# Kernel tuning notes

Measured on AMD Instinct MI355X. Metric: run time of the kernel, lower is better.

The kernel has to match this reference:

```python
import jax, jax.numpy as jnp
import numpy as np

S, T, D_OUT = 64, 256, 64
B = 64
HEADS = 2
D0 = S + T              # 320
D1 = D0 * (1 + HEADS)   # 960
D2 = D1 * (1 + HEADS)   # 2880
PARAM_SCALE = 0.02


def setup_inputs() -> dict:
    key = jax.random.key(0)
    k1, k2, k3, k4 = jax.random.split(key, 4)
    x = jax.random.normal(k1, (B, T, S), dtype=jnp.float32)
    A0 = jax.random.normal(k2, (HEADS, D0, D0), dtype=jnp.float32) * PARAM_SCALE
    A1 = jax.random.normal(k3, (HEADS, D1, D1), dtype=jnp.float32) * PARAM_SCALE
    Wo = jax.random.normal(k4, (D_OUT, D2), dtype=jnp.float32) * PARAM_SCALE
    return {"x": x, "A0": A0, "A1": A1, "Wo": Wo}


def _causal_self_attention(h, A):
    # h: [B, T, d], A: [H, d, d]
    Bsz, Tlen, d = h.shape
    H = A.shape[0]
    # bilinear scores per head: h @ A[i] @ h^T, vectorized over heads
    scores = jnp.einsum('btd,hde,bse->bhts', h, A, h)  # [B, H, T, T]
    neg_inf = jnp.asarray(float('-inf'), dtype=h.dtype)
    mask = jnp.triu(jnp.full((Tlen, Tlen), neg_inf, dtype=h.dtype), k=1)
    attn = jax.nn.softmax(scores + mask, axis=-1)
    out = jnp.einsum('bhts,bsd->bthd', attn, h)  # [B, T, H, d]
    return out.reshape(Bsz, Tlen, H * d)


def reference(x, A0, A1, Wo):
    Bsz, Tlen, _ = x.shape
    # one-hot positional encoding concatenated onto input
    pos = jnp.broadcast_to(jnp.eye(Tlen, dtype=x.dtype)[None], (Bsz, Tlen, Tlen))
    h = jnp.concatenate([x, pos], axis=-1)          # [B, T, S+T]
    h = jnp.concatenate([h, _causal_self_attention(h, A0)], axis=-1)  # [B, T, D1]
    h = jnp.concatenate([h, _causal_self_attention(h, A1)], axis=-1)  # [B, T, D2]
    logits = jnp.einsum('btd,od->bto', h, Wo)       # [B, T, d_out]
    return logits
```

## Files before the change

kernel.cpp:

```cpp
#include <hip/hip_runtime.h>
#include <math.h>

#define NB 64
#define NT 256
#define NS 64
#define ND0 320
#define ND1 960
#define ND2 2880
#define NH 2
#define DC 704

typedef __attribute__((ext_vector_type(8))) _Float16 f16x8;
typedef __attribute__((ext_vector_type(4))) float f32x4;
typedef __attribute__((ext_vector_type(4))) short short4v;

typedef const __attribute__((address_space(1))) void* gas_ptr;
typedef __attribute__((address_space(3))) void* las_ptr;
#define GLOAD16(g, l) __builtin_amdgcn_global_load_lds((gas_ptr)(g), (las_ptr)(l), 16, 0, 0)
#define MFMAH(a, b, c) __builtin_amdgcn_mfma_f32_16x16x32_f16((a), (b), (c), 0, 0, 0)

__device__ __forceinline__ short f2h(float v) {
    union { _Float16 h; short s; } u; u.h = (_Float16)v; return u.s;
}
__device__ __forceinline__ float h2f(short b) {
    union { _Float16 h; short s; } u; u.s = b; return (float)u.h;
}
__device__ __forceinline__ int swz(int o) { return o ^ (((o >> 7) & 7) << 4); }

__global__ __launch_bounds__(256, 2) void gemmG1(
    const short* __restrict__ hc,
    const short* __restrict__ At,
    short* __restrict__ G,
    const float* __restrict__ A1)
{
    int wg = blockIdx.x;
    int q8 = gridDim.x >> 3;
    int sid = (wg & 7) * q8 + (wg >> 3);
    int bx = sid % 15, by = sid / 15;
    int m0 = by << 8, n0 = bx << 7;

    __shared__ short lds[24576];
    int tid = threadIdx.x;
    int lane = tid & 63, w = tid >> 6;
    int wm = w >> 1, wn = w & 1;
    int q = lane >> 4, l15 = lane & 15;

    const short* aS[8]; const short* bS[4];
    int dA[8], dB[4];
#pragma unroll
    for (int j = 0; j < 8; ++j) {
        int o = j * 4096 + tid * 16;
        int c = swz(o); int r = c >> 7, col = (c & 127) >> 1;
        aS[j] = hc + (long)(m0 + r) * DC + col;
        dA[j] = o >> 1;
    }
#pragma unroll
    for (int j = 0; j < 4; ++j) {
        int o = j * 4096 + tid * 16;
        int c = swz(o); int r = c >> 7, col = (c & 127) >> 1;
        bS[j] = At + (long)(n0 + r) * DC + col;
        dB[j] = o >> 1;
    }

    int oa[8][2], ob[4][2];
#pragma unroll
    for (int mf = 0; mf < 8; ++mf)
#pragma unroll
        for (int kf = 0; kf < 2; ++kf) {
            int row = wm * 128 + mf * 16 + l15;
            oa[mf][kf] = swz(row * 128 + (kf * 32 + (q << 3)) * 2) >> 1;
        }
#pragma unroll
    for (int nf = 0; nf < 4; ++nf)
#pragma unroll
        for (int kf = 0; kf < 2; ++kf) {
            int row = wn * 64 + nf * 16 + l15;
            ob[nf][kf] = swz(row * 128 + (kf * 32 + (q << 3)) * 2) >> 1;
        }

    f32x4 acc[8][4] = {};

    for (int k0 = 0; k0 < DC; k0 += 64) {
#pragma unroll
        for (int j = 0; j < 8; ++j) { GLOAD16(aS[j], lds + dA[j]); aS[j] += 64; }
#pragma unroll
        for (int j = 0; j < 4; ++j) { GLOAD16(bS[j], lds + 16384 + dB[j]); bS[j] += 64; }
        __syncthreads();
#pragma unroll
        for (int kf = 0; kf < 2; ++kf) {
            f16x8 vb[4];
#pragma unroll
            for (int nf = 0; nf < 4; ++nf)
                vb[nf] = *(const f16x8*)(lds + 16384 + ob[nf][kf]);
#pragma unroll
            for (int mf = 0; mf < 8; ++mf) {
                f16x8 va = *(const f16x8*)(lds + oa[mf][kf]);
#pragma unroll
                for (int nf = 0; nf < 4; ++nf)
                    acc[mf][nf] = MFMAH(va, vb[nf], acc[mf][nf]);
            }
        }
        __syncthreads();
    }

#pragma unroll
    for (int mf = 0; mf < 8; ++mf)
#pragma unroll
        for (int nf = 0; nf < 4; ++nf) {
            int col = n0 + wn * 64 + nf * 16 + l15;
            int head = (col >= 960) ? 1 : 0;
            int colh = col - head * 960;
            const float* bA = A1 + (long)head * 921600 + colh;
            int rowb = m0 + wm * 128 + mf * 16 + (q << 2);
#pragma unroll
            for (int r = 0; r < 4; ++r) {
                int t = (rowb + r) & 255;
                float f = acc[mf][nf][r] + bA[(long)(64 + t) * 960];
                G[(long)(rowb + r) * 1920 + col] = f2h(f);
            }
        }
}

template <int CMODE, int TERMS, bool AJUMP>
__global__ __launch_bounds__(256, 3) void gemm128(
    const short* Ah, int lda, long sA,
    const short* Bh, const short* Bl, int ldb, long sB,
    float* Cf, int ldcf, long sCf,
    const short* biasH, long ldbias,
    long hsA, long hsC,
    int K)
{
    int bx = blockIdx.x, by = blockIdx.y;
    int m0 = by * 128, n0 = bx * 128;
    if (CMODE == 0 && n0 > m0 + 127) return;
    long zLo = blockIdx.z & 63, zHi = blockIdx.z >> 6;
    const short* pAh = Ah + zLo * sA + zHi * hsA;
    const short* pBh = Bh + zLo * sB;
    const short* pBl = (TERMS == 2) ? (Bl + zLo * sB) : nullptr;

    __shared__ short lds[8192 * (1 + TERMS)];
    short* LAh = lds;
    short* LBh = lds + 8192;
    short* LBl = lds + 16384;

    int tid = threadIdx.x;
    int lane = tid & 63, w = tid >> 6;
    int wr = w >> 1, wc = w & 1;

    const short* aSH[4]; const short* bSH[4]; const short* bSL[4];
    int aLo[4], bLo[4];
#pragma unroll
    for (int j = 0; j < 4; ++j) {
        int o = j * 4096 + tid * 16;
        int c = swz(o); int r = c >> 7, col = (c & 127) >> 1;
        aSH[j] = pAh + (long)(m0 + r) * lda + col;
        aLo[j] = o >> 1;
        bSH[j] = pBh + (long)(n0 + r) * ldb + col;
        if (TERMS == 2) bSL[j] = pBl + (long)(n0 + r) * ldb + col;
        bLo[j] = o >> 1;
    }

    int oa[4][2], ob[4][2];
#pragma unroll
    for (int mf = 0; mf < 4; ++mf)
#pragma unroll
        for (int kf = 0; kf < 2; ++kf) {
            int row = wr * 64 + mf * 16 + (lane & 15);
            oa[mf][kf] = swz(row * 128 + (kf * 32 + ((lane >> 4) << 3)) * 2) >> 1;
        }
#pragma unroll
    for (int nf = 0; nf < 4; ++nf)
#pragma unroll
        for (int kf = 0; kf < 2; ++kf) {
            int row = wc * 64 + nf * 16 + (lane & 15);
            ob[nf][kf] = swz(row * 128 + (kf * 32 + ((lane >> 4) << 3)) * 2) >> 1;
        }

    f32x4 acc[4][4] = {};

    for (int k0 = 0; k0 < K; k0 += 64) {
        int step = (AJUMP && k0 == 0) ? 320 : 64;
#pragma unroll
        for (int j = 0; j < 4; ++j) {
            GLOAD16(aSH[j], LAh + aLo[j]);
            aSH[j] += step;
            GLOAD16(bSH[j], LBh + bLo[j]);
            bSH[j] += 64;
            if (TERMS == 2) { GLOAD16(bSL[j], LBl + bLo[j]); bSL[j] += 64; }
        }
        __syncthreads();
#pragma unroll
        for (int kf = 0; kf < 2; ++kf) {
            f16x8 vbh[4], vbl[4];
#pragma unroll
            for (int nf = 0; nf < 4; ++nf) {
                vbh[nf] = *(const f16x8*)(LBh + ob[nf][kf]);
                if (TERMS == 2) vbl[nf] = *(const f16x8*)(LBl + ob[nf][kf]);
            }
#pragma unroll
            for (int mf = 0; mf < 4; ++mf) {
                f16x8 vah = *(const f16x8*)(LAh + oa[mf][kf]);
#pragma unroll
                for (int nf = 0; nf < 4; ++nf) {
                    acc[mf][nf] = MFMAH(vah, vbh[nf], acc[mf][nf]);
                    if (TERMS == 2) acc[mf][nf] = MFMAH(vah, vbl[nf], acc[mf][nf]);
                }
            }
        }
        __syncthreads();
    }

#pragma unroll
    for (int mf = 0; mf < 4; ++mf)
#pragma unroll
        for (int nf = 0; nf < 4; ++nf) {
            f32x4 v = acc[mf][nf];
            int col  = n0 + wc * 64 + nf * 16 + (lane & 15);
            int rowb = m0 + wr * 64 + mf * 16 + ((lane >> 4) << 2);
#pragma unroll
            for (int r = 0; r < 4; ++r) {
                long o = (zLo * 256 + rowb + r) * ldbias + 64 + col + zHi * hsA;
                v[r] += h2f(biasH[o]);
            }
#pragma unroll
            for (int r = 0; r < 4; ++r)
                Cf[zLo * sCf + zHi * hsC + (long)(rowb + r) * ldcf + col] = v[r];
        }
}

template <int BMODE, int TERMS, bool KCAUSAL, bool ACC, bool OUTU, bool BJUMP>
__global__ __launch_bounds__(256) void gemm_mfma(
    const short* Ah, int lda, long sA,
    const short* Bh, const short* Bl, int ldb, long sB, long hsB,
    float* Cf, int ldcf, long sCf,
    short* Chi, short* Clo, int ldch, long sCh,
    const float* biasF, long ldbias, long hsBias,
    long hsA, long hsC,
    short* UThi,
    int K)
{
    int m0 = blockIdx.y * 128, n0 = blockIdx.x * 64;
    long zLo = blockIdx.z & 63, zHi = blockIdx.z >> 6;
    const short* pAh = Ah + zLo * sA + zHi * hsA;
    const short* pBh = Bh + zLo * sB + zHi * hsB;
    const short* pBl = (TERMS == 2) ? (Bl + zLo * sB + zHi * hsB) : nullptr;

    __shared__ short lds[8192 + TERMS * 4096];
    short* LAh = lds;
    short* LBh = lds + 8192;
    short* LBl = lds + 12288;

    int tid = threadIdx.x;
    int lane = tid & 63, w = tid >> 6;
    int wr = w >> 1, wc = w & 1;

    const short* aSH[4]; const short* bSH[2]; const short* bSL[2];
    int aLo[4], bLo[2];
#pragma unroll
    for (int j = 0; j < 4; ++j) {
        int o = j * 4096 + tid * 16;
        int c = swz(o); int r = c >> 7, col = (c & 127) >> 1;
        aSH[j] = pAh + (long)(m0 + r) * lda + col;
        aLo[j] = o >> 1;
    }
#pragma unroll
    for (int j = 0; j < 2; ++j) {
        int o = j * 4096 + tid * 16;
        int c = swz(o); int r = c >> 7, col = (c & 127) >> 1;
        bSH[j] = pBh + (long)(n0 + r) * ldb + col;
        if (TERMS == 2) bSL[j] = pBl + (long)(n0 + r) * ldb + col;
        bLo[j] = o >> 1;
    }

    int oa[4][2], ob[2][2];
#pragma unroll
    for (int mf = 0; mf < 4; ++mf)
#pragma unroll
        for (int kf = 0; kf < 2; ++kf) {
            int row = wr * 64 + mf * 16 + (lane & 15);
            oa[mf][kf] = swz(row * 128 + (kf * 32 + ((lane >> 4) << 3)) * 2) >> 1;
        }
#pragma unroll
    for (int nf = 0; nf < 2; ++nf)
#pragma unroll
        for (int kf = 0; kf < 2; ++kf) {
            int row = wc * 32 + nf * 16 + (lane & 15);
            ob[nf][kf] = swz(row * 128 + (kf * 32 + ((lane >> 4) << 3)) * 2) >> 1;
        }

    f32x4 acc[4][2] = {};
    int Klim = KCAUSAL ? (K < m0 + 128 ? K : m0 + 128) : K;

    for (int k0 = 0; k0 < Klim; k0 += 64) {
#pragma unroll
        for (int j = 0; j < 4; ++j) {
            GLOAD16(aSH[j], LAh + aLo[j]);
            aSH[j] += 64;
        }
        long bstep = (BJUMP && k0 == 192) ? (1048576L - 192L) : 64L;
#pragma unroll
        for (int j = 0; j < 2; ++j) {
            GLOAD16(bSH[j], LBh + bLo[j]);
            bSH[j] += bstep;
            if (TERMS == 2) { GLOAD16(bSL[j], LBl + bLo[j]); bSL[j] += bstep; }
        }
        __syncthreads();
#pragma unroll
        for (int kf = 0; kf < 2; ++kf) {
            f16x8 vbh[2], vbl[2];
#pragma unroll
            for (int nf = 0; nf < 2; ++nf) {
                vbh[nf] = *(const f16x8*)(LBh + ob[nf][kf]);
                if (TERMS == 2) vbl[nf] = *(const f16x8*)(LBl + ob[nf][kf]);
            }
#pragma unroll
            for (int mf = 0; mf < 4; ++mf) {
                f16x8 vah = *(const f16x8*)(LAh + oa[mf][kf]);
#pragma unroll
                for (int nf = 0; nf < 2; ++nf) {
                    acc[mf][nf] = MFMAH(vah, vbh[nf], acc[mf][nf]);
                    if (TERMS == 2) acc[mf][nf] = MFMAH(vah, vbl[nf], acc[mf][nf]);
                }
            }
        }
        __syncthreads();
    }

#pragma unroll
    for (int mf = 0; mf < 4; ++mf)
#pragma unroll
        for (int nf = 0; nf < 2; ++nf) {
            f32x4 v = acc[mf][nf];
            int col  = n0 + wc * 32 + nf * 16 + (lane & 15);
            int rowb = m0 + wr * 64 + mf * 16 + ((lane >> 4) << 2);
            if (BMODE == 1) {
#pragma unroll
                for (int r = 0; r < 4; ++r) {
                    int t = (rowb + r) & 255;
                    v[r] += biasF[zLo * hsBias + (long)(64 + t) * ldbias + col];
                }
            } else if (BMODE == 3) {
#pragma unroll
                for (int r = 0; r < 4; ++r) {
                    int t = (rowb + r) & 255;
                    v[r] += biasF[(long)(col - n0) * 2880 + (n0 >> 6) * 960 + 64 + t];
                }
            }
            if (OUTU) {
                if (n0 == 0) {
#pragma unroll
                    for (int r = 0; r < 4; ++r)
                        Cf[(long)(rowb + r) * ldcf + col] = v[r];
                } else {
                    int head = (n0 >> 6) - 1;
                    int o = col - n0;
                    short hs[4];
#pragma unroll
                    for (int r = 0; r < 4; ++r) hs[r] = f2h(v[r]);
                    short4v th = {hs[0], hs[1], hs[2], hs[3]};
                    *(short4v*)(UThi + head * 1048576L + (long)o * 16384 + rowb) = th;
                }
            } else if (ACC) {
#pragma unroll
                for (int r = 0; r < 4; ++r)
                    Cf[zLo * sCf + (long)(rowb + r) * ldcf + col] += v[r];
            } else if (Cf) {
#pragma unroll
                for (int r = 0; r < 4; ++r)
                    Cf[zLo * sCf + (long)(rowb + r) * ldcf + col] = v[r];
            } else {
#pragma unroll
                for (int r = 0; r < 4; ++r) {
                    float f = v[r];
                    short hi = f2h(f);
                    Chi[zHi * hsC + zLo * sCh + (long)(rowb + r) * ldch + col] = hi;
                    if (Clo)
                        Clo[zHi * hsC + zLo * sCh + (long)(rowb + r) * ldch + col] = f2h(f - h2f(hi));
                }
            }
        }
}

__global__ __launch_bounds__(256) void build_h_rows(const float* __restrict__ x,
                                                    short* __restrict__ hhi) {
    int idx = blockIdx.x * 256 + threadIdx.x;
    int bt = idx >> 6, c = idx & 63;
    hhi[(long)bt * DC + c] = f2h(x[(long)bt * NS + c]);
}

__global__ __launch_bounds__(256) void build_hT_x(const float* __restrict__ x,
                                                  short* __restrict__ hTh) {
    __shared__ float tile[32][33];
    int c0 = blockIdx.x * 32, t0 = blockIdx.y * 32, b = blockIdx.z;
    int tx = threadIdx.x, ty = threadIdx.y;
    const float* xb = x + (long)b * NT * NS;
#pragma unroll
    for (int i = ty; i < 32; i += 8) tile[i][tx] = xb[(long)(t0 + i) * NS + c0 + tx];
    __syncthreads();
    long base = (long)b * (NS * 256);
#pragma unroll
    for (int i = ty; i < 32; i += 8)
        hTh[base + (long)(c0 + i) * 256 + t0 + tx] = f2h(tile[tx][i]);
}

__global__ void build_At(const float* __restrict__ A,
                         short* __restrict__ hi,
                         int dN, int dK, int srcLd, int shift, int dSrcN) {
    __shared__ float tile[32][33];
    int k0 = blockIdx.x * 32, n0 = blockIdx.y * 32;
    long hbase = (long)blockIdx.z * srcLd * srcLd;
    int tx = threadIdx.x, ty = threadIdx.y;
#pragma unroll
    for (int i = ty; i < 32; i += 8) {
        int k = k0 + i;
        int srck = (k < 64) ? k : k + shift;
        tile[i][tx] = (n0 + tx < dSrcN) ? A[hbase + (long)srck * srcLd + n0 + tx] : 0.f;
    }
    __syncthreads();
    long obase = (long)blockIdx.z * dN * dK;
#pragma unroll
    for (int i = ty; i < 32; i += 8)
        hi[obase + (long)(n0 + i) * dK + k0 + tx] = f2h(tile[tx][i]);
}

__global__ __launch_bounds__(256) void build_Wf(const float* __restrict__ Wo,
                                                short* __restrict__ hi) {
    int idx = blockIdx.x * 256 + threadIdx.x;
    if (idx >= 192 * DC) return;
    int r = idx / DC, kc = idx - r * DC;
    int o = r & 63, chunk = r >> 6;
    int srck = (kc < 64) ? kc : kc + 256;
    hi[idx] = f2h(Wo[(long)o * ND2 + chunk * 960 + srck]);
}

__global__ __launch_bounds__(256) void softmax_split(const float* S,
                                                     short* pHi,
                                                     int ldo, long hs) {
    int row  = blockIdx.x * 4 + (threadIdx.x >> 6);
    int t    = row & (NT - 1);
    int hrow = row & 16383;
    int head = row >> 14;
    int lane = threadIdx.x & 63;
    int s0   = lane << 2;
    const float* p = S + (long)row * NT;

    float4 v = *(const float4*)(p + s0);
    float vv[4] = {v.x, v.y, v.z, v.w};
    float mx = -INFINITY;
#pragma unroll
    for (int j = 0; j < 4; ++j)
        if (s0 + j <= t) mx = fmaxf(mx, vv[j]);
    for (int off = 32; off; off >>= 1) mx = fmaxf(mx, __shfl_down(mx, off));
    mx = __shfl(mx, 0);

    float e[4]; float sum = 0.f;
#pragma unroll
    for (int j = 0; j < 4; ++j) {
        e[j] = (s0 + j <= t) ? __expf(vv[j] - mx) : 0.f;
        sum += e[j];
    }
    for (int off = 32; off; off >>= 1) sum += __shfl_down(sum, off);
    sum = __shfl(sum, 0);
    float inv = 1.f / sum;

    short hsv[4];
#pragma unroll
    for (int j = 0; j < 4; ++j) hsv[j] = f2h(e[j] * inv);
    short4v hv = {hsv[0], hsv[1], hsv[2], hsv[3]};
    *(short4v*)(pHi + (long)head * hs + (long)hrow * ldo + s0) = hv;
}

__global__ __launch_bounds__(256) void build_h0(const float* __restrict__ x,
                                                float* __restrict__ h) {
    int idx = blockIdx.x * 256 + threadIdx.x;
    int bt = idx / ND0;
    int c  = idx - bt * ND0;
    int t  = bt & (NT - 1);
    float v;
    if (c < NS) v = x[(long)bt * NS + c];
    else        v = ((c - NS) == t) ? 1.0f : 0.0f;
    h[(long)bt * ND2 + c] = v;
}

template <bool BT, bool CAUSAL>
__global__ __launch_bounds__(256) void gemm64(
    const float* __restrict__ A, int lda, long sA,
    const float* __restrict__ Bm, int ldb, long sB,
    float* __restrict__ C, int ldc, long sC, int K)
{
    int m0 = blockIdx.y * 64, n0 = blockIdx.x * 64;
    if (CAUSAL && n0 > m0 + 63) return;
    long z = blockIdx.z;
    A += z * sA; Bm += z * sB; C += z * sC;

    __shared__ float As[16][68];
    __shared__ float Bs[16][68];

    int tid = threadIdx.x;
    int tx = tid & 15, ty = tid >> 4;
    int rowA = tid >> 2, kA = (tid & 3) << 2;
    int kB = tid >> 4,  colB = (tid & 15) << 2;

    float acc[4][4] = {};

    for (int k0 = 0; k0 < K; k0 += 16) {
        float4 av = *(const float4*)(A + (long)(m0 + rowA) * lda + k0 + kA);
        As[kA + 0][rowA] = av.x; As[kA + 1][rowA] = av.y;
        As[kA + 2][rowA] = av.z; As[kA + 3][rowA] = av.w;
        if (BT) {
            float4 bv = *(const float4*)(Bm + (long)(n0 + rowA) * ldb + k0 + kA);
            Bs[kA + 0][rowA] = bv.x; Bs[kA + 1][rowA] = bv.y;
            Bs[kA + 2][rowA] = bv.z; Bs[kA + 3][rowA] = bv.w;
        } else {
            float4 bv = *(const float4*)(Bm + (long)(k0 + kB) * ldb + n0 + colB);
            *(float4*)(&Bs[kB][colB]) = bv;
        }
        __syncthreads();
#pragma unroll
        for (int kk = 0; kk < 16; ++kk) {
            float4 a4 = *(const float4*)(&As[kk][ty << 2]);
            float4 b4 = *(const float4*)(&Bs[kk][tx << 2]);
            float a[4] = {a4.x, a4.y, a4.z, a4.w};
            float b[4] = {b4.x, b4.y, b4.z, b4.w};
#pragma unroll
            for (int i = 0; i < 4; ++i)
#pragma unroll
                for (int j = 0; j < 4; ++j)
                    acc[i][j] += a[i] * b[j];
        }
        __syncthreads();
    }
#pragma unroll
    for (int i = 0; i < 4; ++i) {
        float4 v = {acc[i][0], acc[i][1], acc[i][2], acc[i][3]};
        *(float4*)(C + (long)(m0 + (ty << 2) + i) * ldc + n0 + (tx << 2)) = v;
    }
}

__global__ __launch_bounds__(256) void softmax_causal(float* __restrict__ P) {
    int row  = blockIdx.x * 4 + (threadIdx.x >> 6);
    int t    = row & (NT - 1);
    int lane = threadIdx.x & 63;
    int s0   = lane << 2;
    float* p = P + (long)row * NT;

    float4 v = *(const float4*)(p + s0);
    float vv[4] = {v.x, v.y, v.z, v.w};
    float mx = -INFINITY;
#pragma unroll
    for (int j = 0; j < 4; ++j)
        if (s0 + j <= t) mx = fmaxf(mx, vv[j]);
    for (int off = 32; off; off >>= 1) mx = fmaxf(mx, __shfl_down(mx, off));
    mx = __shfl(mx, 0);

    float e[4]; float sum = 0.f;
#pragma unroll
    for (int j = 0; j < 4; ++j) {
        e[j] = (s0 + j <= t) ? __expf(vv[j] - mx) : 0.f;
        sum += e[j];
    }
    for (int off = 32; off; off >>= 1) sum += __shfl_down(sum, off);
    sum = __shfl(sum, 0);
    float inv = 1.f / sum;
    float4 o = {e[0] * inv, e[1] * inv, e[2] * inv, e[3] * inv};
    *(float4*)(p + s0) = o;
}

extern "C" void kernel_launch(void* const* d_in, const int* in_sizes, int n_in,
                              void* d_out, int out_size, void* d_ws, size_t ws_size,
                              hipStream_t stream) {
    const float* x  = (const float*)d_in[0];
    const float* A0 = (const float*)d_in[1];
    const float* A1 = (const float*)d_in[2];
    const float* Wo = (const float*)d_in[3];
    float* out = (float*)d_out;

    if (ws_size >= 175120384UL) {
        char* wsb = (char*)d_ws;
        short* hc_hi = (short*)(wsb);
        short* G_hi  = (short*)(wsb + 46137344L);
        float* S     = (float*)(wsb + 113246208L);
        short* P     = (short*)(wsb + 146800640L);
        short* hT_hi = (short*)(wsb + 163577856L);
        short* At_hi = (short*)(wsb + 167772160L);
        short* Wf_hi = (short*)(wsb + 170655744L);
        short* UT_hi = (short*)(wsb + 170926080L);

        build_h_rows<<<4096, 256, 0, stream>>>(x, hc_hi);
        build_hT_x<<<dim3(2, 8, 64), dim3(32, 8), 0, stream>>>(x, hT_hi);
        build_Wf<<<528, 256, 0, stream>>>(Wo, Wf_hi);

        build_At<<<dim3(2, 10, 2), dim3(32, 8), 0, stream>>>(A0, At_hi, ND0, 64, ND0, 0, ND0);
        gemm_mfma<1, 1, false, false, false, false><<<dim3(5, 128, 2), 256, 0, stream>>>(
            hc_hi, DC, 0L,
            At_hi, nullptr, 64, 20480L, 0L,
            nullptr, 0, 0L, G_hi, nullptr, 640, 320L,
            A0, 320L, 102400L,
            0L, 0L,
            nullptr, 64);
        gemm128<0, 1, false><<<dim3(2, 2, 128), 256, 0, stream>>>(
            G_hi, 640, 163840L,
            hc_hi, nullptr, DC, 180224L,
            S, NT, 65536L,
            G_hi, 640L,
            320L, 4194304L, 64);
        softmax_split<<<8192, 256, 0, stream>>>(S, hc_hi + 128, DC, 320L);
        gemm_mfma<0, 1, true, false, false, false><<<dim3(1, 2, 128), 256, 0, stream>>>(
            hc_hi + 128, DC, 180224L,
            hT_hi, nullptr, 256, 16384L, 0L,
            nullptr, 0, 0L,
            hc_hi + 64, nullptr, DC, 180224L,
            nullptr, 0L, 0L,
            320L, 320L,
            nullptr, 256);

        gemm_mfma<3, 1, false, false, true, false><<<dim3(3, 128, 1), 256, 0, stream>>>(
            hc_hi, DC, 0L,
            Wf_hi, nullptr, DC, 0L, 0L,
            out, NS, 0L, nullptr, nullptr, 0, 0L,
            Wo, 0L, 0L,
            0L, 0L,
            UT_hi, DC);

        build_At<<<dim3(22, 30, 2), dim3(32, 8), 0, stream>>>(A1, At_hi, 960, DC, ND1, 256, ND1);
        gemmG1<<<960, 256, 0, stream>>>(hc_hi, At_hi, G_hi, A1);
        gemm128<0, 1, true><<<dim3(2, 2, 128), 256, 0, stream>>>(
            G_hi, 1920, 491520L,
            hc_hi, nullptr, DC, 180224L,
            S, NT, 65536L,
            G_hi, 1920L,
            960L, 4194304L, DC);
        softmax_split<<<8192, 256, 0, stream>>>(S, P, 512, 256L);
        gemm_mfma<0, 1, false, true, false, true><<<dim3(1, 2, 64), 256, 0, stream>>>(
            P, 512, 131072L,
            UT_hi, nullptr, 16384, 256L, 0L,
            out, NS, 16384L, nullptr, nullptr, 0, 0L,
            nullptr, 0L, 0L,
            0L, 0L,
            nullptr, 512);
        return;
    }

    float* ws = (float*)d_ws;
    float* h  = ws;
    float* G  = ws + 47185920L;
    float* Pf = ws + 47185920L + 15728640L;

    build_h0<<<(NB * NT * ND0) / 256, 256, 0, stream>>>(x, h);

    for (int layer = 0; layer < 2; ++layer) {
        int d = layer ? ND1 : ND0;
        const float* Am = layer ? A1 : A0;
        for (int head = 0; head < NH; ++head) {
            const float* Ah = Am + (long)head * d * d;
            gemm64<false, false><<<dim3(d / 64, 256, 1), 256, 0, stream>>>(
                h, ND2, 0L, Ah, d, 0L, G, d, 0L, d);
            gemm64<true, true><<<dim3(4, 4, NB), 256, 0, stream>>>(
                G, d, (long)NT * d, h, ND2, (long)NT * ND2,
                Pf, NT, (long)NT * NT, d);
            softmax_causal<<<(NB * NT) / 4, 256, 0, stream>>>(Pf);
            gemm64<false, false><<<dim3(d / 64, 4, NB), 256, 0, stream>>>(
                Pf, NT, (long)NT * NT, h, ND2, (long)NT * ND2,
                h + (long)d * (1 + head), ND2, (long)NT * ND2, NT);
        }
    }
    gemm64<true, false><<<dim3(1, 256, 1), 256, 0, stream>>>(
        h, ND2, 0L, Wo, ND2, 0L, out, NS, 0L, ND2);
}
```

Before: 177.5 us.

## Double-buffer gemmG1, store scores in fp16, fuse setup kernels, drop split-term paths

gemmG1 now stages K in 32-wide chunks into two LDS buffers and prefetches the next chunk while MFMAs run on the current one, which removes one barrier per step and hides load latency. Attention scores S are written and read as fp16 instead of fp32, halving the score traffic between the GEMM and softmax. The four setup kernels (h rows, x transpose, Wf, A0 transpose) are merged into one launch to cut launch overhead, and the unused lo-term template paths are removed. Storing scores in fp16 adds rounding before softmax, and large logits could lose accuracy or overflow.

```diff
diff --git a/kernel.cpp b/kernel.cpp
--- a/kernel.cpp
+++ b/kernel.cpp
@@ -45,63 +45,69 @@
     int wm = w >> 1, wn = w & 1;
     int q = lane >> 4, l15 = lane & 15;
 
-    const short* aS[8]; const short* bS[4];
-    int dA[8], dB[4];
-#pragma unroll
-    for (int j = 0; j < 8; ++j) {
-        int o = j * 4096 + tid * 16;
-        int c = swz(o); int r = c >> 7, col = (c & 127) >> 1;
-        aS[j] = hc + (long)(m0 + r) * DC + col;
-        dA[j] = o >> 1;
-    }
+    const short* aS[4]; const short* bS[2];
+    int dA[4], dB[2];
 #pragma unroll
     for (int j = 0; j < 4; ++j) {
         int o = j * 4096 + tid * 16;
-        int c = swz(o); int r = c >> 7, col = (c & 127) >> 1;
-        bS[j] = At + (long)(n0 + r) * DC + col;
+        int c = swz(o);
+        int sr = c >> 7, byt = c & 127;
+        int row = sr * 2 + (byt >> 6), k = (byt & 63) >> 1;
+        aS[j] = hc + (long)(m0 + row) * DC + k;
+        dA[j] = o >> 1;
+    }
+#pragma unroll
+    for (int j = 0; j < 2; ++j) {
+        int o = j * 4096 + tid * 16;
+        int c = swz(o);
+        int sr = c >> 7, byt = c & 127;
+        int row = sr * 2 + (byt >> 6), k = (byt & 63) >> 1;
+        bS[j] = At + (long)(n0 + row) * DC + k;
         dB[j] = o >> 1;
     }
 
-    int oa[8][2], ob[4][2];
-#pragma unroll
-    for (int mf = 0; mf < 8; ++mf)
-#pragma unroll
-        for (int kf = 0; kf < 2; ++kf) {
-            int row = wm * 128 + mf * 16 + l15;
-            oa[mf][kf] = swz(row * 128 + (kf * 32 + (q << 3)) * 2) >> 1;
-        }
-#pragma unroll
-    for (int nf = 0; nf < 4; ++nf)
-#pragma unroll
-        for (int kf = 0; kf < 2; ++kf) {
-            int row = wn * 64 + nf * 16 + l15;
-            ob[nf][kf] = swz(row * 128 + (kf * 32 + (q << 3)) * 2) >> 1;
-        }
+#define STG(BUF) { \
+    GLOAD16(aS[0], lds + (BUF) + dA[0]); GLOAD16(aS[1], lds + (BUF) + dA[1]); \
+    GLOAD16(aS[2], lds + (BUF) + dA[2]); GLOAD16(aS[3], lds + (BUF) + dA[3]); \
+    GLOAD16(bS[0], lds + (BUF) + 8192 + dB[0]); GLOAD16(bS[1], lds + (BUF) + 8192 + dB[1]); \
+    aS[0] += 32; aS[1] += 32; aS[2] += 32; aS[3] += 32; bS[0] += 32; bS[1] += 32; }
+
+    int oa[8], ob[4];
+#pragma unroll
+    for (int mf = 0; mf < 8; ++mf) {
+        int row = wm * 128 + mf * 16 + l15;
+        int sr = row >> 1, half = row & 1;
+        oa[mf] = swz(sr * 128 + half * 64 + q * 16) >> 1;
+    }
+#pragma unroll
+    for (int nf = 0; nf < 4; ++nf) {
+        int row = wn * 64 + nf * 16 + l15;
+        int sr = row >> 1, half = row & 1;
+        ob[nf] = swz(sr * 128 + half * 64 + q * 16) >> 1;
+    }
 
     f32x4 acc[8][4] = {};
 
-    for (int k0 = 0; k0 < DC; k0 += 64) {
-#pragma unroll
-        for (int j = 0; j < 8; ++j) { GLOAD16(aS[j], lds + dA[j]); aS[j] += 64; }
-#pragma unroll
-        for (int j = 0; j < 4; ++j) { GLOAD16(bS[j], lds + 16384 + dB[j]); bS[j] += 64; }
-        __syncthreads();
-#pragma unroll
-        for (int kf = 0; kf < 2; ++kf) {
-            f16x8 vb[4];
+    STG(0)
+    __syncthreads();
+#pragma unroll 2
+    for (int t = 0; t < 22; ++t) {
+        int cur = (t & 1) * 12288;
+        if (t < 21) STG(12288 - cur)
+        f16x8 vb[4];
+#pragma unroll
+        for (int nf = 0; nf < 4; ++nf)
+            vb[nf] = *(const f16x8*)(lds + cur + 8192 + ob[nf]);
+#pragma unroll
+        for (int mf = 0; mf < 8; ++mf) {
+            f16x8 va = *(const f16x8*)(lds + cur + oa[mf]);
 #pragma unroll
             for (int nf = 0; nf < 4; ++nf)
-                vb[nf] = *(const f16x8*)(lds + 16384 + ob[nf][kf]);
-#pragma unroll
-            for (int mf = 0; mf < 8; ++mf) {
-                f16x8 va = *(const f16x8*)(lds + oa[mf][kf]);
-#pragma unroll
-                for (int nf = 0; nf < 4; ++nf)
-                    acc[mf][nf] = MFMAH(va, vb[nf], acc[mf][nf]);
-            }
-        }
-        __syncthreads();
-    }
+                acc[mf][nf] = MFMAH(va, vb[nf], acc[mf][nf]);
+        }
+        __syncthreads();
+    }
+#undef STG
 
 #pragma unroll
     for (int mf = 0; mf < 8; ++mf)
@@ -121,33 +127,31 @@
         }
 }
 
-template <int CMODE, int TERMS, bool AJUMP>
+template <bool AJUMP>
 __global__ __launch_bounds__(256, 3) void gemm128(
     const short* Ah, int lda, long sA,
-    const short* Bh, const short* Bl, int ldb, long sB,
-    float* Cf, int ldcf, long sCf,
+    const short* Bh, int ldb, long sB,
+    short* Sf, int ldcf, long sCf,
     const short* biasH, long ldbias,
     long hsA, long hsC,
     int K)
 {
     int bx = blockIdx.x, by = blockIdx.y;
     int m0 = by * 128, n0 = bx * 128;
-    if (CMODE == 0 && n0 > m0 + 127) return;
+    if (n0 > m0 + 127) return;
     long zLo = blockIdx.z & 63, zHi = blockIdx.z >> 6;
     const short* pAh = Ah + zLo * sA + zHi * hsA;
     const short* pBh = Bh + zLo * sB;
-    const short* pBl = (TERMS == 2) ? (Bl + zLo * sB) : nullptr;
-
-    __shared__ short lds[8192 * (1 + TERMS)];
+
+    __shared__ short lds[16384];
     short* LAh = lds;
     short* LBh = lds + 8192;
-    short* LBl = lds + 16384;
 
     int tid = threadIdx.x;
     int lane = tid & 63, w = tid >> 6;
     int wr = w >> 1, wc = w & 1;
 
-    const short* aSH[4]; const short* bSH[4]; const short* bSL[4];
+    const short* aSH[4]; const short* bSH[4];
     int aLo[4], bLo[4];
 #pragma unroll
     for (int j = 0; j < 4; ++j) {
@@ -156,7 +160,6 @@
         aSH[j] = pAh + (long)(m0 + r) * lda + col;
         aLo[j] = o >> 1;
         bSH[j] = pBh + (long)(n0 + r) * ldb + col;
-        if (TERMS == 2) bSL[j] = pBl + (long)(n0 + r) * ldb + col;
         bLo[j] = o >> 1;
     }
 
@@ -186,25 +189,20 @@
             aSH[j] += step;
             GLOAD16(bSH[j], LBh + bLo[j]);
             bSH[j] += 64;
-            if (TERMS == 2) { GLOAD16(bSL[j], LBl + bLo[j]); bSL[j] += 64; }
         }
         __syncthreads();
 #pragma unroll
         for (int kf = 0; kf < 2; ++kf) {
-            f16x8 vbh[4], vbl[4];
-#pragma unroll
-            for (int nf = 0; nf < 4; ++nf) {
+            f16x8 vbh[4];
+#pragma unroll
+            for (int nf = 0; nf < 4; ++nf)
                 vbh[nf] = *(const f16x8*)(LBh + ob[nf][kf]);
-                if (TERMS == 2) vbl[nf] = *(const f16x8*)(LBl + ob[nf][kf]);
-            }
 #pragma unroll
             for (int mf = 0; mf < 4; ++mf) {
                 f16x8 vah = *(const f16x8*)(LAh + oa[mf][kf]);
 #pragma unroll
-                for (int nf = 0; nf < 4; ++nf) {
+                for (int nf = 0; nf < 4; ++nf)
                     acc[mf][nf] = MFMAH(vah, vbh[nf], acc[mf][nf]);
-                    if (TERMS == 2) acc[mf][nf] = MFMAH(vah, vbl[nf], acc[mf][nf]);
-                }
             }
         }
         __syncthreads();
@@ -224,16 +222,16 @@
             }
 #pragma unroll
             for (int r = 0; r < 4; ++r)
-                Cf[zLo * sCf + zHi * hsC + (long)(rowb + r) * ldcf + col] = v[r];
-        }
-}
-
-template <int BMODE, int TERMS, bool KCAUSAL, bool ACC, bool OUTU, bool BJUMP>
+                Sf[zLo * sCf + zHi * hsC + (long)(rowb + r) * ldcf + col] = f2h(v[r]);
+        }
+}
+
+template <int BMODE, bool KCAUSAL, bool ACC, bool OUTU, bool BJUMP>
 __global__ __launch_bounds__(256) void gemm_mfma(
     const short* Ah, int lda, long sA,
-    const short* Bh, const short* Bl, int ldb, long sB, long hsB,
+    const short* Bh, int ldb, long sB, long hsB,
     float* Cf, int ldcf, long sCf,
-    short* Chi, short* Clo, int ldch, long sCh,
+    short* Chi, int ldch, long sCh,
     const float* biasF, long ldbias, long hsBias,
     long hsA, long hsC,
     short* UThi,
@@ -243,18 +241,16 @@
     long zLo = blockIdx.z & 63, zHi = blockIdx.z >> 6;
     const short* pAh = Ah + zLo * sA + zHi * hsA;
     const short* pBh = Bh + zLo * sB + zHi * hsB;
-    const short* pBl = (TERMS == 2) ? (Bl + zLo * sB + zHi * hsB) : nullptr;
-
-    __shared__ short lds[8192 + TERMS * 4096];
+
+    __shared__ short lds[12288];
     short* LAh = lds;
     short* LBh = lds + 8192;
-    short* LBl = lds + 12288;
 
     int tid = threadIdx.x;
     int lane = tid & 63, w = tid >> 6;
     int wr = w >> 1, wc = w & 1;
 
-    const short* aSH[4]; const short* bSH[2]; const short* bSL[2];
+    const short* aSH[4]; const short* bSH[2];
     int aLo[4], bLo[2];
 #pragma unroll
     for (int j = 0; j < 4; ++j) {
@@ -268,7 +264,6 @@
         int o = j * 4096 + tid * 16;
         int c = swz(o); int r = c >> 7, col = (c & 127) >> 1;
         bSH[j] = pBh + (long)(n0 + r) * ldb + col;
-        if (TERMS == 2) bSL[j] = pBl + (long)(n0 + r) * ldb + col;
         bLo[j] = o >> 1;
     }
 
@@ -302,25 +297,20 @@
         for (int j = 0; j < 2; ++j) {
             GLOAD16(bSH[j], LBh + bLo[j]);
             bSH[j] += bstep;
-            if (TERMS == 2) { GLOAD16(bSL[j], LBl + bLo[j]); bSL[j] += bstep; }
         }
         __syncthreads();
 #pragma unroll
         for (int kf = 0; kf < 2; ++kf) {
-            f16x8 vbh[2], vbl[2];
-#pragma unroll
-            for (int nf = 0; nf < 2; ++nf) {
+            f16x8 vbh[2];
+#pragma unroll
+            for (int nf = 0; nf < 2; ++nf)
                 vbh[nf] = *(const f16x8*)(LBh + ob[nf][kf]);
-                if (TERMS == 2) vbl[nf] = *(const f16x8*)(LBl + ob[nf][kf]);
-            }
 #pragma unroll
             for (int mf = 0; mf < 4; ++mf) {
                 f16x8 vah = *(const f16x8*)(LAh + oa[mf][kf]);
 #pragma unroll
-                for (int nf = 0; nf < 2; ++nf) {
+                for (int nf = 0; nf < 2; ++nf)
                     acc[mf][nf] = MFMAH(vah, vbh[nf], acc[mf][nf]);
-                    if (TERMS == 2) acc[mf][nf] = MFMAH(vah, vbl[nf], acc[mf][nf]);
-                }
             }
         }
         __syncthreads();
@@ -370,37 +360,62 @@
                     Cf[zLo * sCf + (long)(rowb + r) * ldcf + col] = v[r];
             } else {
 #pragma unroll
-                for (int r = 0; r < 4; ++r) {
-                    float f = v[r];
-                    short hi = f2h(f);
-                    Chi[zHi * hsC + zLo * sCh + (long)(rowb + r) * ldch + col] = hi;
-                    if (Clo)
-                        Clo[zHi * hsC + zLo * sCh + (long)(rowb + r) * ldch + col] = f2h(f - h2f(hi));
-                }
+                for (int r = 0; r < 4; ++r)
+                    Chi[zHi * hsC + zLo * sCh + (long)(rowb + r) * ldch + col] = f2h(v[r]);
             }
         }
 }
 
-__global__ __launch_bounds__(256) void build_h_rows(const float* __restrict__ x,
-                                                    short* __restrict__ hhi) {
-    int idx = blockIdx.x * 256 + threadIdx.x;
-    int bt = idx >> 6, c = idx & 63;
-    hhi[(long)bt * DC + c] = f2h(x[(long)bt * NS + c]);
-}
-
-__global__ __launch_bounds__(256) void build_hT_x(const float* __restrict__ x,
-                                                  short* __restrict__ hTh) {
+__global__ __launch_bounds__(256) void build_all(const float* __restrict__ x,
+                                                 const float* __restrict__ Wo,
+                                                 const float* __restrict__ A0,
+                                                 short* __restrict__ hc,
+                                                 short* __restrict__ hT,
+                                                 short* __restrict__ Wf,
+                                                 short* __restrict__ At0) {
     __shared__ float tile[32][33];
-    int c0 = blockIdx.x * 32, t0 = blockIdx.y * 32, b = blockIdx.z;
-    int tx = threadIdx.x, ty = threadIdx.y;
-    const float* xb = x + (long)b * NT * NS;
-#pragma unroll
-    for (int i = ty; i < 32; i += 8) tile[i][tx] = xb[(long)(t0 + i) * NS + c0 + tx];
-    __syncthreads();
-    long base = (long)b * (NS * 256);
-#pragma unroll
-    for (int i = ty; i < 32; i += 8)
-        hTh[base + (long)(c0 + i) * 256 + t0 + tx] = f2h(tile[tx][i]);
+    int blk = blockIdx.x;
+    int tid = threadIdx.x;
+    if (blk < 4096) {
+        int idx = blk * 256 + tid;
+        int bt = idx >> 6, c = idx & 63;
+        hc[(long)bt * DC + c] = f2h(x[(long)bt * NS + c]);
+    } else if (blk < 5120) {
+        int i = blk - 4096;
+        int c0 = (i & 1) * 32, t0 = ((i >> 1) & 7) * 32, b = i >> 4;
+        int tx = tid & 31, ty = tid >> 5;
+        const float* xb = x + (long)b * NT * NS;
+#pragma unroll
+        for (int ii = ty; ii < 32; ii += 8) tile[ii][tx] = xb[(long)(t0 + ii) * NS + c0 + tx];
+        __syncthreads();
+        long base = (long)b * (NS * 256);
+#pragma unroll
+        for (int ii = ty; ii < 32; ii += 8)
+            hT[base + (long)(c0 + ii) * 256 + t0 + tx] = f2h(tile[tx][ii]);
+    } else if (blk < 5648) {
+        int idx = (blk - 5120) * 256 + tid;
+        if (idx < 192 * DC) {
+            int r = idx / DC, kc = idx - r * DC;
+            int o = r & 63, chunk = r >> 6;
+            int srck = (kc < 64) ? kc : kc + 256;
+            Wf[idx] = f2h(Wo[(long)o * ND2 + chunk * 960 + srck]);
+        }
+    } else {
+        int i = blk - 5648;
+        int k0 = (i & 1) * 32;
+        int n0 = ((i >> 1) % 10) * 32;
+        int z  = i / 20;
+        int tx = tid & 31, ty = tid >> 5;
+        long hbase = (long)z * ND0 * ND0;
+#pragma unroll
+        for (int ii = ty; ii < 32; ii += 8)
+            tile[ii][tx] = A0[hbase + (long)(k0 + ii) * ND0 + n0 + tx];
+        __syncthreads();
+        long obase = (long)z * ND0 * 64;
+#pragma unroll
+        for (int ii = ty; ii < 32; ii += 8)
+            At0[obase + (long)(n0 + ii) * 64 + k0 + tx] = f2h(tile[tx][ii]);
+    }
 }
 
 __global__ void build_At(const float* __restrict__ A,
@@ -423,17 +438,7 @@
         hi[obase + (long)(n0 + i) * dK + k0 + tx] = f2h(tile[tx][i]);
 }
 
-__global__ __launch_bounds__(256) void build_Wf(const float* __restrict__ Wo,
-                                                short* __restrict__ hi) {
-    int idx = blockIdx.x * 256 + threadIdx.x;
-    if (idx >= 192 * DC) return;
-    int r = idx / DC, kc = idx - r * DC;
-    int o = r & 63, chunk = r >> 6;
-    int srck = (kc < 64) ? kc : kc + 256;
-    hi[idx] = f2h(Wo[(long)o * ND2 + chunk * 960 + srck]);
-}
-
-__global__ __launch_bounds__(256) void softmax_split(const float* S,
+__global__ __launch_bounds__(256) void softmax_split(const short* S,
                                                      short* pHi,
                                                      int ldo, long hs) {
     int row  = blockIdx.x * 4 + (threadIdx.x >> 6);
@@ -442,10 +447,10 @@
     int head = row >> 14;
     int lane = threadIdx.x & 63;
     int s0   = lane << 2;
-    const float* p = S + (long)row * NT;
-
-    float4 v = *(const float4*)(p + s0);
-    float vv[4] = {v.x, v.y, v.z, v.w};
+    const short* p = S + (long)row * NT;
+
+    short4v sv = *(const short4v*)(p + s0);
+    float vv[4] = {h2f(sv[0]), h2f(sv[1]), h2f(sv[2]), h2f(sv[3])};
     float mx = -INFINITY;
 #pragma unroll
     for (int j = 0; j < 4; ++j)
@@ -579,62 +584,59 @@
         char* wsb = (char*)d_ws;
         short* hc_hi = (short*)(wsb);
         short* G_hi  = (short*)(wsb + 46137344L);
-        float* S     = (float*)(wsb + 113246208L);
+        short* S     = (short*)(wsb + 113246208L);
         short* P     = (short*)(wsb + 146800640L);
         short* hT_hi = (short*)(wsb + 163577856L);
         short* At_hi = (short*)(wsb + 167772160L);
         short* Wf_hi = (short*)(wsb + 170655744L);
         short* UT_hi = (short*)(wsb + 170926080L);
 
-        build_h_rows<<<4096, 256, 0, stream>>>(x, hc_hi);
-        build_hT_x<<<dim3(2, 8, 64), dim3(32, 8), 0, stream>>>(x, hT_hi);
-        build_Wf<<<528, 256, 0, stream>>>(Wo, Wf_hi);
-
-        build_At<<<dim3(2, 10, 2), dim3(32, 8), 0, stream>>>(A0, At_hi, ND0, 64, ND0, 0, ND0);
-        gemm_mfma<1, 1, false, false, false, false><<<dim3(5, 128, 2), 256, 0, stream>>>(
+        build_all<<<5688, 256, 0, stream>>>(x, Wo, A0, hc_hi, hT_hi, Wf_hi, At_hi);
+
+        gemm_mfma<1, false, false, false, false><<<dim3(5, 128, 2), 256, 0, stream>>>(
             hc_hi, DC, 0L,
-            At_hi, nullptr, 64, 20480L, 0L,
-            nullptr, 0, 0L, G_hi, nullptr, 640, 320L,
+            At_hi, 64, 20480L, 0L,
+            nullptr, 0, 0L, G_hi, 640, 320L,
             A0, 320L, 102400L,
             0L, 0L,
             nullptr, 64);
-        gemm128<0, 1, false><<<dim3(2, 2, 128), 256, 0, stream>>>(
+        gemm128<false><<<dim3(2, 2, 128), 256, 0, stream>>>(
             G_hi, 640, 163840L,
-            hc_hi, nullptr, DC, 180224L,
+            hc_hi, DC, 180224L,
             S, NT, 65536L,
             G_hi, 640L,
             320L, 4194304L, 64);
         softmax_split<<<8192, 256, 0, stream>>>(S, hc_hi + 128, DC, 320L);
-        gemm_mfma<0, 1, true, false, false, false><<<dim3(1, 2, 128), 256, 0, stream>>>(
+        gemm_mfma<0, true, false, false, false><<<dim3(1, 2, 128), 256, 0, stream>>>(
             hc_hi + 128, DC, 180224L,
-            hT_hi, nullptr, 256, 16384L, 0L,
+            hT_hi, 256, 16384L, 0L,
             nullptr, 0, 0L,
-            hc_hi + 64, nullptr, DC, 180224L,
+            hc_hi + 64, DC, 180224L,
             nullptr, 0L, 0L,
             320L, 320L,
             nullptr, 256);
 
-        gemm_mfma<3, 1, false, false, true, false><<<dim3(3, 128, 1), 256, 0, stream>>>(
+        gemm_mfma<3, false, false, true, false><<<dim3(3, 128, 1), 256, 0, stream>>>(
             hc_hi, DC, 0L,
-            Wf_hi, nullptr, DC, 0L, 0L,
-            out, NS, 0L, nullptr, nullptr, 0, 0L,
+            Wf_hi, DC, 0L, 0L,
+            out, NS, 0L, nullptr, 0, 0L,
             Wo, 0L, 0L,
             0L, 0L,
             UT_hi, DC);
 
         build_At<<<dim3(22, 30, 2), dim3(32, 8), 0, stream>>>(A1, At_hi, 960, DC, ND1, 256, ND1);
         gemmG1<<<960, 256, 0, stream>>>(hc_hi, At_hi, G_hi, A1);
-        gemm128<0, 1, true><<<dim3(2, 2, 128), 256, 0, stream>>>(
+        gemm128<true><<<dim3(2, 2, 128), 256, 0, stream>>>(
             G_hi, 1920, 491520L,
-            hc_hi, nullptr, DC, 180224L,
+            hc_hi, DC, 180224L,
             S, NT, 65536L,
             G_hi, 1920L,
             960L, 4194304L, DC);
         softmax_split<<<8192, 256, 0, stream>>>(S, P, 512, 256L);
-        gemm_mfma<0, 1, false, true, false, true><<<dim3(1, 2, 64), 256, 0, stream>>>(
+        gemm_mfma<0, false, true, false, true><<<dim3(1, 2, 64), 256, 0, stream>>>(
             P, 512, 131072L,
-            UT_hi, nullptr, 16384, 256L, 0L,
-            out, NS, 16384L, nullptr, nullptr, 0, 0L,
+            UT_hi, 16384, 256L, 0L,
+            out, NS, 16384L, nullptr, 0, 0L,
             nullptr, 0L, 0L,
             0L, 0L,
             nullptr, 512);
```

After: 172.3 us. 1.03x faster.
